# Performance work log

Hardware: AMD Instinct MI355X
Metric: run time of the kernel (lower is better)

Reference implementation:

```python
import jax, jax.numpy as jnp
import numpy as np


def setup_inputs() -> dict:
    key = jax.random.key(0)
    k1, k2, k3, k4 = jax.random.split(key, 4)
    B, Q, K, H, D = 2, 2048, 2048, 16, 64
    qs = jax.random.normal(k1, (B, Q, H, D), dtype=jnp.float32)
    ks = jax.random.normal(k2, (B, K, H, D), dtype=jnp.float32)
    vs = jax.random.normal(k3, (B, K, H, D), dtype=jnp.float32)
    # valid lengths in [1, K] so no row is fully masked
    valid_lens = jnp.maximum(jax.random.randint(k4, (B,), 0, K + 1, dtype=jnp.int32), 1)
    return {"qs": qs, "ks": ks, "vs": vs, "valid_lens": valid_lens}


def reference(qs, ks, vs, valid_lens):
    # Faithful math of ScanAttention: scaled dot-product attention with a
    # per-batch key-validity mask (online-softmax scan == exact softmax).
    B, Q, H, D = qs.shape
    K = ks.shape[1]
    scale = 1.0 / jnp.sqrt(jnp.float32(D))
    # [B, H, Q, K]
    scores = jnp.einsum('bqhd,bkhd->bhqk', qs * scale, ks)
    ks_mask = jnp.arange(K)[None, :] < valid_lens[:, None]  # [B, K]
    scores = jnp.where(ks_mask[:, None, None, :], scores, -jnp.inf)
    attn = jax.nn.softmax(scores, axis=-1)
    out = jnp.einsum('bhqk,bkhd->bqhd', attn, vs)  # [B, Q, H, D]
    return out
```

## Files before the change

kernel.cpp:

```cpp
#include <hip/hip_runtime.h>
#include <hip/hip_bf16.h>

typedef __bf16 bf16t;
typedef bf16t bf16x4 __attribute__((ext_vector_type(4)));
typedef bf16t bf16x8 __attribute__((ext_vector_type(8)));
typedef float f32x2 __attribute__((ext_vector_type(2)));
typedef float f32x4 __attribute__((ext_vector_type(4)));
typedef float f32x16 __attribute__((ext_vector_type(16)));
typedef unsigned short u16x8 __attribute__((ext_vector_type(8)));
typedef unsigned int u32x4 __attribute__((ext_vector_type(4)));

#define NB 2
#define NQ 2048
#define NK 2048
#define NH 16
#define ND 64
#define HD (NH * ND)
#define KVBLK 64
#define NUNITS 512
#define SCALE_LOG2E 0.18033688011112042f
#define RESCALE_THR 8.0f

#define OPART_BYTES(n) ((size_t)(n) * 8388608ULL)
#define ML_BYTES(n)    ((size_t)(n) * 524288ULL)

__device__ inline unsigned cvt_pk_bf16(float a, float b) {
    unsigned r;
    asm("v_cvt_pk_bf16_f32 %0, %1, %2" : "=v"(r) : "v"(a), "v"(b));
    return r;
}

__device__ inline void plswap(unsigned& a, unsigned& b) {
#if __has_builtin(__builtin_amdgcn_permlane32_swap)
    auto r = __builtin_amdgcn_permlane32_swap(a, b, false, false);
    a = r[0]; b = r[1];
#else
    const unsigned as = __shfl_xor((int)a, 32);
    const unsigned bs = __shfl_xor((int)b, 32);
    const bool lh = (threadIdx.x & 32) != 0;
    const unsigned na = lh ? bs : a;
    const unsigned nb = lh ? b : as;
    a = na; b = nb;
#endif
}

template <int NSPLIT>
__global__ __launch_bounds__(256) __attribute__((amdgpu_waves_per_eu(3)))
void scan_attn(const float* __restrict__ qs, const float* __restrict__ ks,
               const float* __restrict__ vs, const int* __restrict__ vlen,
               float* __restrict__ out, char* __restrict__ ws)
{
    const int bid = blockIdx.x;
    const int x    = bid & 7;
    const int jj   = bid >> 3;
    const int b    = jj & 1;
    const int code = x | ((jj >> 1) << 3);
    const int qt   = code / (16 * NSPLIT);
    const int rr   = code % (16 * NSPLIT);
    const int h    = rr / NSPLIT;
    const int s    = rr % NSPLIT;
    const int uidx = ((b * NH + h) << 4) + qt;

    const int tid  = threadIdx.x;
    const int wq   = tid >> 6;
    const int lane = tid & 63;
    const int ql   = lane & 31;
    const int lh   = lane >> 5;
    const int swq  = (ql & 7) << 4;
    const int q    = qt * 128 + wq * 32 + ql;

    const int nkv    = vlen[b];
    const int ntiles = (nkv + KVBLK - 1) >> 6;
    const int rem    = nkv & 63;
    const int tlo    = (ntiles * s) / NSPLIT;
    const int thi    = (ntiles * (s + 1)) / NSPLIT;

    const float* qptr = qs + ((size_t)b * NQ + q) * HD + h * ND;
    const float* kptr = ks + (size_t)b * NK * HD + h * ND;
    const float* vptr = vs + (size_t)b * NK * HD + h * ND;

    __shared__ __align__(16) char smem[2][16384];

    bf16x8 qf[4];
#pragma unroll
    for (int c = 0; c < 4; ++c) {
        const float* p = qptr + 16 * c + 8 * lh;
        f32x4 lo4 = *reinterpret_cast<const f32x4*>(p);
        f32x4 hi4 = *reinterpret_cast<const f32x4*>(p + 4);
#pragma unroll
        for (int e = 0; e < 4; ++e) {
            qf[c][e]     = (bf16t)(lo4[e] * SCALE_LOG2E);
            qf[c][4 + e] = (bf16t)(hi4[e] * SCALE_LOG2E);
        }
    }

    const int skr  = tid >> 3;
    const int skc  = (tid & 7) << 3;
    const int skc2 = (tid & 7) << 4;
    const int ksw  = (skr & 7) << 4;
    const int svd  = tid & 63;
    const int svk8 = (tid >> 6) << 3;
    const int svk2 = (tid >> 6) << 4;
    const int vsw  = (svd & 7) << 4;

    f32x4 kreg[2];
    float vreg[8];

    auto load_half = [&](int kb, int half) {
        const float* kp = kptr + (size_t)(kb + half * 32 + skr) * HD + skc;
        kreg[0] = *reinterpret_cast<const f32x4*>(kp);
        kreg[1] = *reinterpret_cast<const f32x4*>(kp + 4);
        const float* vp = vptr + (size_t)(kb + half * 32 + svk8) * HD + svd;
#pragma unroll
        for (int e = 0; e < 8; ++e)
            vreg[e] = vp[(size_t)e * HD];
    };

    auto store_half = [&](int buf, int half) {
        u16x8 w0;
#pragma unroll
        for (int i = 0; i < 2; ++i)
#pragma unroll
            for (int e = 0; e < 4; ++e)
                w0[4 * i + e] = __builtin_bit_cast(unsigned short, (bf16t)kreg[i][e]);
        char* kb_ = smem[buf] + (half * 32 + skr) * 128;
        *reinterpret_cast<u16x8*>(kb_ + (skc2 ^ ksw)) = w0;

        u16x8 x0;
#pragma unroll
        for (int e = 0; e < 8; ++e)
            x0[e] = __builtin_bit_cast(unsigned short, (bf16t)vreg[e]);
        char* vb_ = smem[buf] + 8192 + svd * 128;
        *reinterpret_cast<u16x8*>(vb_ + ((svk2 + half * 64) ^ vsw)) = x0;
    };

    float mrun = -__builtin_inff();
    float lrun = 0.0f;
    f32x16 o[2] = {};

    if (tlo < thi) {
        load_half(tlo << 6, 0); store_half(0, 0);
        load_half(tlo << 6, 1); store_half(0, 1);
    }
    __syncthreads();

    int cur = 0;
    for (int t = tlo; t < thi; ++t) {
        const int kb = t << 6;
        const bool has_next = (t + 1) < thi;
        if (has_next) load_half((t + 1) << 6, 0);

        const char* kbuf = smem[cur];
        const char* vbuf = smem[cur] + 8192;

#pragma unroll
        for (int h2 = 0; h2 < 2; ++h2) {
            f32x16 s_ = {};
            const char* krow = kbuf + (32 * h2 + ql) * 128;
#pragma unroll
            for (int c = 0; c < 4; ++c) {
                bf16x8 kf = *reinterpret_cast<const bf16x8*>(
                    krow + ((32 * c + 16 * lh) ^ swq));
                s_ = __builtin_amdgcn_mfma_f32_32x32x16_bf16(kf, qf[c], s_, 0, 0, 0);
            }

            if (rem && t == ntiles - 1) {
                const int krem = nkv - kb;
#pragma unroll
                for (int r = 0; r < 16; ++r)
                    if (32 * h2 + (r & 3) + 8 * (r >> 2) + 4 * lh >= krem)
                        s_[r] = -__builtin_inff();
            }

            float pmax = -__builtin_inff();
#pragma unroll
            for (int r = 0; r < 16; ++r) pmax = fmaxf(pmax, s_[r]);
            pmax = fmaxf(pmax, __shfl_xor(pmax, 32));

            if (!__all(pmax <= mrun + RESCALE_THR)) {
                const float mnew  = fmaxf(mrun, pmax);
                const float alpha = exp2f(mrun - mnew);
                lrun *= alpha;
                o[0] *= alpha;
                o[1] *= alpha;
                mrun = mnew;
            }

            float ps = 0.0f;
#pragma unroll
            for (int r = 0; r < 16; ++r) {
                const float pv = exp2f(s_[r] - mrun);
                s_[r] = pv;
                ps += pv;
            }
            ps += __shfl_xor(ps, 32);
            lrun += ps;

            bf16x8 pf[2];
#pragma unroll
            for (int cc = 0; cc < 2; ++cc) {
                const int r0 = cc * 8;
                unsigned a0 = cvt_pk_bf16(s_[r0 + 0], s_[r0 + 1]);
                unsigned b0 = cvt_pk_bf16(s_[r0 + 4], s_[r0 + 5]);
                plswap(a0, b0);
                unsigned a1 = cvt_pk_bf16(s_[r0 + 2], s_[r0 + 3]);
                unsigned b1 = cvt_pk_bf16(s_[r0 + 6], s_[r0 + 7]);
                plswap(a1, b1);
                pf[cc] = __builtin_bit_cast(bf16x8, (u32x4){a0, a1, b0, b1});
            }

#pragma unroll
            for (int dt = 0; dt < 2; ++dt) {
                const char* vrow = vbuf + (32 * dt + ql) * 128;
#pragma unroll
                for (int cc = 0; cc < 2; ++cc) {
                    const int c = 2 * h2 + cc;
                    bf16x8 vf = *reinterpret_cast<const bf16x8*>(
                        vrow + ((32 * c + 16 * lh) ^ swq));
                    o[dt] = __builtin_amdgcn_mfma_f32_32x32x16_bf16(vf, pf[cc], o[dt], 0, 0, 0);
                }
            }

            if (h2 == 0 && has_next) {
                store_half(cur ^ 1, 0);
                load_half((t + 1) << 6, 1);
            }
        }

        if (has_next) store_half(cur ^ 1, 1);
        __syncthreads();
        cur ^= 1;
    }

    if (NSPLIT == 1) {
        const float inv = 1.0f / lrun;
        float* op = out + ((size_t)b * NQ + q) * HD + h * ND;
#pragma unroll
        for (int dt = 0; dt < 2; ++dt)
#pragma unroll
            for (int rg = 0; rg < 4; ++rg) {
                f32x4 w;
#pragma unroll
                for (int e = 0; e < 4; ++e) w[e] = o[dt][4 * rg + e] * inv;
                *reinterpret_cast<f32x4*>(op + 32 * dt + 8 * rg + 4 * lh) = w;
            }
    } else {
        const int p = uidx * NSPLIT + s;
        bf16t* op = (bf16t*)ws + ((size_t)p * 128 + wq * 32 + ql) * 64;
#pragma unroll
        for (int dt = 0; dt < 2; ++dt)
#pragma unroll
            for (int rg = 0; rg < 4; ++rg) {
                bf16x4 w;
#pragma unroll
                for (int e = 0; e < 4; ++e) w[e] = (bf16t)o[dt][4 * rg + e];
                *reinterpret_cast<bf16x4*>(op + 32 * dt + 8 * rg + 4 * lh) = w;
            }
        if (lh == 0) {
            f32x2* ml = (f32x2*)(ws + OPART_BYTES(NSPLIT));
            ml[p * 128 + wq * 32 + ql] = (f32x2){mrun, lrun};
        }
    }
}

template <int NSPLIT>
__global__ __launch_bounds__(256)
void merge_attn(const char* __restrict__ ws, float* __restrict__ out)
{
    const int u  = blockIdx.x;
    const int b  = u >> 8;
    const int h  = (u >> 4) & 15;
    const int qt = u & 15;
    const int tid = threadIdx.x;
    const int q  = tid >> 1;
    const int dh = (tid & 1) * 32;

    const bf16t* opart = (const bf16t*)ws;
    const f32x2* ml    = (const f32x2*)(ws + OPART_BYTES(NSPLIT));

    float m_s[NSPLIT], l_s[NSPLIT];
    float M = -__builtin_inff();
#pragma unroll
    for (int s = 0; s < NSPLIT; ++s) {
        f32x2 v = ml[(u * NSPLIT + s) * 128 + q];
        m_s[s] = v[0]; l_s[s] = v[1];
        M = fmaxf(M, v[0]);
    }
    float L = 0.0f, w_s[NSPLIT];
#pragma unroll
    for (int s = 0; s < NSPLIT; ++s) {
        w_s[s] = exp2f(m_s[s] - M);
        L += w_s[s] * l_s[s];
    }
    const float inv = 1.0f / L;

    float acc[32];
#pragma unroll
    for (int e = 0; e < 32; ++e) acc[e] = 0.0f;
#pragma unroll
    for (int s = 0; s < NSPLIT; ++s) {
        const bf16t* op = opart + ((size_t)(u * NSPLIT + s) * 128 + q) * 64 + dh;
#pragma unroll
        for (int c = 0; c < 4; ++c) {
            bf16x8 v8 = *reinterpret_cast<const bf16x8*>(op + 8 * c);
#pragma unroll
            for (int e = 0; e < 8; ++e)
                acc[8 * c + e] += w_s[s] * (float)v8[e];
        }
    }

    float* op = out + ((size_t)b * NQ + qt * 128 + q) * HD + h * ND + dh;
#pragma unroll
    for (int c = 0; c < 8; ++c) {
        f32x4 st;
#pragma unroll
        for (int e = 0; e < 4; ++e) st[e] = acc[4 * c + e] * inv;
        *reinterpret_cast<f32x4*>(op + 4 * c) = st;
    }
}

extern "C" void kernel_launch(void* const* d_in, const int* in_sizes, int n_in,
                              void* d_out, int out_size, void* d_ws, size_t ws_size,
                              hipStream_t stream)
{
    const float* qs   = (const float*)d_in[0];
    const float* ks   = (const float*)d_in[1];
    const float* vs   = (const float*)d_in[2];
    const int*   vlen = (const int*)d_in[3];
    float* out = (float*)d_out;
    char*  ws  = (char*)d_ws;

    const size_t need2 = OPART_BYTES(2) + ML_BYTES(2);

    if (ws_size >= need2) {
        scan_attn<2><<<NUNITS * 2, 256, 0, stream>>>(qs, ks, vs, vlen, out, ws);
        merge_attn<2><<<NUNITS, 256, 0, stream>>>(ws, out);
    } else {
        scan_attn<1><<<NUNITS, 256, 0, stream>>>(qs, ks, vs, vlen, out, ws);
    }
}
```

Measured before the change: 68.29 us.

## Precompute bf16 swizzled K and transposed V, stage via global_load_lds

Adds pre-pass kernels that convert K to bf16 in a swizzled row layout and V to a transposed swizzled bf16 layout in workspace. The attention kernel then stages tiles directly into LDS with global_load_lds, removing per-block fp32 loads, conversions and strided V gathers. This costs two extra kernel launches and a full extra pass over K/V memory. If the workspace is too small, no kernel computes the output.

New measurement: 79.20 us. 1.16x slower.

```diff
diff --git a/kernel.cpp b/kernel.cpp
--- a/kernel.cpp
+++ b/kernel.cpp
@@ -21,6 +21,9 @@
 #define SCALE_LOG2E 0.18033688011112042f
 #define RESCALE_THR 8.0f
 
+#define KWS_BYTES  8388608ULL
+#define PRE_BYTES  16777216ULL
+#define HEAD_BYTES 262144ULL
 #define OPART_BYTES(n) ((size_t)(n) * 8388608ULL)
 #define ML_BYTES(n)    ((size_t)(n) * 524288ULL)
 
@@ -44,10 +47,78 @@
 #endif
 }
 
+__device__ inline void gl_lds16(const void* g, void* l) {
+    __builtin_amdgcn_global_load_lds(
+        (const __attribute__((address_space(1))) unsigned int*)g,
+        (__attribute__((address_space(3))) unsigned int*)l, 16, 0, 0);
+}
+
+__global__ __launch_bounds__(256)
+void prep_k(const float* __restrict__ ks, char* __restrict__ ws)
+{
+    const int g    = blockIdx.x * 256 + threadIdx.x;
+    const int c8   = g & 7;
+    const int row  = g >> 3;
+    const int k    = row & 2047;
+    const int head = row >> 11;
+    const int b    = head >> 4;
+    const int h    = head & 15;
+
+    const int y  = c8 << 4;
+    const int d2 = y ^ ((k & 7) << 4);
+    const int e0 = d2 >> 1;
+
+    const float* src = ks + (((size_t)b * NK + k) * NH + h) * ND + e0;
+    f32x4 lo = *reinterpret_cast<const f32x4*>(src);
+    f32x4 hi = *reinterpret_cast<const f32x4*>(src + 4);
+    u16x8 o;
+#pragma unroll
+    for (int e = 0; e < 4; ++e) {
+        o[e]     = __builtin_bit_cast(unsigned short, (bf16t)lo[e]);
+        o[4 + e] = __builtin_bit_cast(unsigned short, (bf16t)hi[e]);
+    }
+    *reinterpret_cast<u16x8*>(ws + (size_t)row * 128 + y) = o;
+}
+
+__global__ __launch_bounds__(256)
+void prep_v(const float* __restrict__ vs, char* __restrict__ ws)
+{
+    __shared__ __align__(16) unsigned short lt[64][64];
+
+    const int bid = blockIdx.x;
+    const int kt  = bid & 31;
+    const int h   = (bid >> 5) & 15;
+    const int b   = bid >> 9;
+    const int tid = threadIdx.x;
+
+    const int kr = tid >> 2;
+    const int c4 = tid & 3;
+    const float* src = vs + (((size_t)b * NK + kt * 64 + kr) * NH + h) * ND + c4 * 16;
+#pragma unroll
+    for (int i = 0; i < 4; ++i) {
+        f32x4 v = *reinterpret_cast<const f32x4*>(src + 4 * i);
+#pragma unroll
+        for (int e = 0; e < 4; ++e)
+            lt[c4 * 16 + 4 * i + e][kr] =
+                __builtin_bit_cast(unsigned short, (bf16t)v[e]);
+    }
+    __syncthreads();
+
+    char* dst = ws + KWS_BYTES + (size_t)(b * NH + h) * HEAD_BYTES;
+#pragma unroll
+    for (int r = 0; r < 2; ++r) {
+        const int L = r * 4096 + tid * 16;
+        const int d = L >> 7;
+        const int y = L & 127;
+        u16x8 v = *reinterpret_cast<const u16x8*>(
+            (const char*)lt + d * 128 + (y ^ ((d & 7) << 4)));
+        *reinterpret_cast<u16x8*>(dst + (size_t)d * 4096 + kt * 128 + y) = v;
+    }
+}
+
 template <int NSPLIT>
-__global__ __launch_bounds__(256) __attribute__((amdgpu_waves_per_eu(3)))
-void scan_attn(const float* __restrict__ qs, const float* __restrict__ ks,
-               const float* __restrict__ vs, const int* __restrict__ vlen,
+__global__ __launch_bounds__(256)
+void scan_attn(const float* __restrict__ qs, const int* __restrict__ vlen,
                float* __restrict__ out, char* __restrict__ ws)
 {
     const int bid = blockIdx.x;
@@ -76,8 +147,9 @@
     const int thi    = (ntiles * (s + 1)) / NSPLIT;
 
     const float* qptr = qs + ((size_t)b * NQ + q) * HD + h * ND;
-    const float* kptr = ks + (size_t)b * NK * HD + h * ND;
-    const float* vptr = vs + (size_t)b * NK * HD + h * ND;
+    const size_t hoff = (size_t)(b * NH + h) * HEAD_BYTES;
+    const char*  kws  = ws + hoff;
+    const char*  vtws = ws + KWS_BYTES + hoff;
 
     __shared__ __align__(16) char smem[2][16384];
 
@@ -94,61 +166,31 @@
         }
     }
 
-    const int skr  = tid >> 3;
-    const int skc  = (tid & 7) << 3;
-    const int skc2 = (tid & 7) << 4;
-    const int ksw  = (skr & 7) << 4;
-    const int svd  = tid & 63;
-    const int svk8 = (tid >> 6) << 3;
-    const int svk2 = (tid >> 6) << 4;
-    const int vsw  = (svd & 7) << 4;
-
-    f32x4 kreg[2];
-    float vreg[8];
-
-    auto load_half = [&](int kb, int half) {
-        const float* kp = kptr + (size_t)(kb + half * 32 + skr) * HD + skc;
-        kreg[0] = *reinterpret_cast<const f32x4*>(kp);
-        kreg[1] = *reinterpret_cast<const f32x4*>(kp + 4);
-        const float* vp = vptr + (size_t)(kb + half * 32 + svk8) * HD + svd;
-#pragma unroll
-        for (int e = 0; e < 8; ++e)
-            vreg[e] = vp[(size_t)e * HD];
-    };
-
-    auto store_half = [&](int buf, int half) {
-        u16x8 w0;
-#pragma unroll
-        for (int i = 0; i < 2; ++i)
-#pragma unroll
-            for (int e = 0; e < 4; ++e)
-                w0[4 * i + e] = __builtin_bit_cast(unsigned short, (bf16t)kreg[i][e]);
-        char* kb_ = smem[buf] + (half * 32 + skr) * 128;
-        *reinterpret_cast<u16x8*>(kb_ + (skc2 ^ ksw)) = w0;
-
-        u16x8 x0;
-#pragma unroll
-        for (int e = 0; e < 8; ++e)
-            x0[e] = __builtin_bit_cast(unsigned short, (bf16t)vreg[e]);
-        char* vb_ = smem[buf] + 8192 + svd * 128;
-        *reinterpret_cast<u16x8*>(vb_ + ((svk2 + half * 64) ^ vsw)) = x0;
+    auto stage = [&](int buf, int kb) {
+        const char* ks_ = kws + (size_t)kb * 128;
+        const char* vs_ = vtws + (size_t)kb * 2;
+        char* kd = smem[buf];
+        char* vd = smem[buf] + 8192;
+#pragma unroll
+        for (int r = 0; r < 2; ++r) {
+            const int L = r * 4096 + tid * 16;
+            gl_lds16(ks_ + L, kd + L);
+            gl_lds16(vs_ + (size_t)(L >> 7) * 4096 + (L & 127), vd + L);
+        }
     };
 
     float mrun = -__builtin_inff();
     float lrun = 0.0f;
     f32x16 o[2] = {};
 
-    if (tlo < thi) {
-        load_half(tlo << 6, 0); store_half(0, 0);
-        load_half(tlo << 6, 1); store_half(0, 1);
-    }
+    if (tlo < thi) stage(0, tlo << 6);
     __syncthreads();
 
     int cur = 0;
     for (int t = tlo; t < thi; ++t) {
         const int kb = t << 6;
         const bool has_next = (t + 1) < thi;
-        if (has_next) load_half((t + 1) << 6, 0);
+        if (has_next) stage(cur ^ 1, (t + 1) << 6);
 
         const char* kbuf = smem[cur];
         const char* vbuf = smem[cur] + 8192;
@@ -220,18 +262,13 @@
                     o[dt] = __builtin_amdgcn_mfma_f32_32x32x16_bf16(vf, pf[cc], o[dt], 0, 0, 0);
                 }
             }
-
-            if (h2 == 0 && has_next) {
-                store_half(cur ^ 1, 0);
-                load_half((t + 1) << 6, 1);
-            }
-        }
-
-        if (has_next) store_half(cur ^ 1, 1);
+        }
+
         __syncthreads();
         cur ^= 1;
     }
 
+    char* part = ws + PRE_BYTES;
     if (NSPLIT == 1) {
         const float inv = 1.0f / lrun;
         float* op = out + ((size_t)b * NQ + q) * HD + h * ND;
@@ -246,7 +283,7 @@
             }
     } else {
         const int p = uidx * NSPLIT + s;
-        bf16t* op = (bf16t*)ws + ((size_t)p * 128 + wq * 32 + ql) * 64;
+        bf16t* op = (bf16t*)part + ((size_t)p * 128 + wq * 32 + ql) * 64;
 #pragma unroll
         for (int dt = 0; dt < 2; ++dt)
 #pragma unroll
@@ -257,7 +294,7 @@
                 *reinterpret_cast<bf16x4*>(op + 32 * dt + 8 * rg + 4 * lh) = w;
             }
         if (lh == 0) {
-            f32x2* ml = (f32x2*)(ws + OPART_BYTES(NSPLIT));
+            f32x2* ml = (f32x2*)(part + OPART_BYTES(NSPLIT));
             ml[p * 128 + wq * 32 + ql] = (f32x2){mrun, lrun};
         }
     }
@@ -265,7 +302,7 @@
 
 template <int NSPLIT>
 __global__ __launch_bounds__(256)
-void merge_attn(const char* __restrict__ ws, float* __restrict__ out)
+void merge_attn(const char* __restrict__ part, float* __restrict__ out)
 {
     const int u  = blockIdx.x;
     const int b  = u >> 8;
@@ -275,8 +312,8 @@
     const int q  = tid >> 1;
     const int dh = (tid & 1) * 32;
 
-    const bf16t* opart = (const bf16t*)ws;
-    const f32x2* ml    = (const f32x2*)(ws + OPART_BYTES(NSPLIT));
+    const bf16t* opart = (const bf16t*)part;
+    const f32x2* ml    = (const f32x2*)(part + OPART_BYTES(NSPLIT));
 
     float m_s[NSPLIT], l_s[NSPLIT];
     float M = -__builtin_inff();
@@ -330,12 +367,16 @@
     float* out = (float*)d_out;
     char*  ws  = (char*)d_ws;
 
-    const size_t need2 = OPART_BYTES(2) + ML_BYTES(2);
+    const size_t need2 = PRE_BYTES + OPART_BYTES(2) + ML_BYTES(2);
+    const size_t need1 = PRE_BYTES;
+
+    prep_k<<<2048, 256, 0, stream>>>(ks, ws);
+    prep_v<<<1024, 256, 0, stream>>>(vs, ws);
 
     if (ws_size >= need2) {
-        scan_attn<2><<<NUNITS * 2, 256, 0, stream>>>(qs, ks, vs, vlen, out, ws);
-        merge_attn<2><<<NUNITS, 256, 0, stream>>>(ws, out);
-    } else {
-        scan_attn<1><<<NUNITS, 256, 0, stream>>>(qs, ks, vs, vlen, out, ws);
-    }
-}
+        scan_attn<2><<<NUNITS * 2, 256, 0, stream>>>(qs, vlen, out, ws);
+        merge_attn<2><<<NUNITS, 256, 0, stream>>>(ws + PRE_BYTES, out);
+    } else if (ws_size >= need1) {
+        scan_attn<1><<<NUNITS, 256, 0, stream>>>(qs, vlen, out, ws);
+    }
+}
```
